# Performance work log

Measured on AMD Instinct MI355X. Metric: run time of the kernel, lower is better.

Reference implementation:

```python
import jax, jax.numpy as jnp
import numpy as np

B, T, D, H = 2, 2048, 1024, 16
DK = D // H


def setup_inputs() -> dict:
    key = jax.random.key(0)
    ks = jax.random.split(key, 12)
    q = jax.random.normal(ks[0], (B, T, D), jnp.float32)
    k = jax.random.normal(ks[1], (B, T, D), jnp.float32)
    v = jax.random.normal(ks[2], (B, T, D), jnp.float32)
    # padding mask [B,1,T]: 1 = valid, 0 = pad (nonzero per torch eq(0) semantics)
    lengths = jnp.array([T, (3 * T) // 4])
    mask = (jnp.arange(T)[None, None, :] < lengths[:, None, None]).astype(jnp.int32)
    s = 0.02
    Wq = jax.random.normal(ks[3], (D, D), jnp.float32) * s
    Wk = jax.random.normal(ks[4], (D, D), jnp.float32) * s
    Wv = jax.random.normal(ks[5], (D, D), jnp.float32) * s
    Wo = jax.random.normal(ks[6], (D, D), jnp.float32) * s
    bq = jnp.zeros((D,), jnp.float32)
    bk = jnp.zeros((D,), jnp.float32)
    bv = jnp.zeros((D,), jnp.float32)
    bo = jnp.zeros((D,), jnp.float32)
    return {"query": q, "key": k, "value": v, "mask": mask,
            "Wq": Wq, "bq": bq, "Wk": Wk, "bk": bk,
            "Wv": Wv, "bv": bv, "Wo": Wo, "bo": bo}


def reference(query, key, value, mask, Wq, bq, Wk, bk, Wv, bv, Wo, bo):
    # q,k,v projections -> [B, H, T, DK]
    def proj(x, W, b):
        return (x @ W.T + b).reshape(B, T, H, DK).transpose(0, 2, 1, 3)
    q = proj(query, Wq, bq)
    k = proj(key, Wk, bk)
    v = proj(value, Wv, bv)
    scores = jnp.einsum("bhqd,bhkd->bhqk", q, k) * (DK ** -0.5)  # [B,H,T,T]
    m = (mask == 0)[:, None, :, :]  # [B,1,1,T] broadcast over heads/queries
    scores = jnp.where(m, -jnp.inf, scores)
    attn = jax.nn.softmax(scores, axis=-1)
    attn = jnp.where(m, 0.0, attn)
    x = jnp.einsum("bhqk,bhkd->bhqd", attn, v)  # [B,H,T,DK]
    x = x.transpose(0, 2, 1, 3).reshape(B, T, D)
    return x @ Wo.T + bo
```

## Files before the change

### kernel.cpp

```cpp
#include <hip/hip_runtime.h>

typedef unsigned short u16;
typedef unsigned int u32;
typedef __bf16 bf16x8 __attribute__((ext_vector_type(8)));
typedef float floatx4 __attribute__((ext_vector_type(4)));

#define BB 2
#define TT 2048
#define DD 1024
#define HH 16
#define DKK 64
#define ACT (BB * TT * DD)
#define WTE (DD * DD)

__device__ inline u16 f2bf(float f) {
    union { float f; u32 u; } c; c.f = f;
    u32 r = (c.u + 0x7fffu + ((c.u >> 16) & 1u)) >> 16;
    return (u16)r;
}
__device__ inline u32 pack2bf(float a, float b) {
    return (u32)f2bf(a) | ((u32)f2bf(b) << 16);
}

typedef __attribute__((address_space(1))) const u32 gas_u32;
typedef __attribute__((address_space(3))) u32 las_u32;
__device__ __forceinline__ void gl2lds16(const u16* g, u16* l) {
    __builtin_amdgcn_global_load_lds((gas_u32*)g, (las_u32*)l, 16, 0, 0);
}

struct CvtArgs { const float* src[7]; u16* dst[7]; };
__global__ __launch_bounds__(256) void convert_bf16(CvtArgs a) {
    int bid = blockIdx.x, t, local;
    if (bid < 768) { t = bid >> 8; local = bid & 255; }
    else { int r = bid - 768; t = 3 + (r >> 6); local = r & 63; }
    const float* s = a.src[t];
    u16* d = a.dst[t];
    const int base = local * 16384;
    for (int i = 0; i < 8; i++) {
        const int idx = base + i * 2048 + threadIdx.x * 8;
        float4 x0 = *(const float4*)(s + idx);
        float4 x1 = *(const float4*)(s + idx + 4);
        uint4 p;
        p.x = pack2bf(x0.x, x0.y); p.y = pack2bf(x0.z, x0.w);
        p.z = pack2bf(x1.x, x1.y); p.w = pack2bf(x1.z, x1.w);
        *(uint4*)(d + idx) = p;
    }
}

__global__ __launch_bounds__(256) void qkv_gemm(
    const u16* __restrict__ Qc, const u16* __restrict__ Kc,
    const u16* __restrict__ Vc,
    const u16* __restrict__ Wqc, const u16* __restrict__ Wkc,
    const u16* __restrict__ Wvc,
    const float* __restrict__ bq, const float* __restrict__ bk,
    const float* __restrict__ bv,
    u16* __restrict__ ws)
{
    __shared__ __align__(16) u16 As[128 * 32];
    __shared__ __align__(16) u16 Bs[128 * 32];
    const int z = blockIdx.z;
    const u16* A = (z == 0) ? Qc : (z == 1) ? Kc : Vc;
    const u16* W = (z == 0) ? Wqc : (z == 1) ? Wkc : Wvc;
    const float* bias = (z == 0) ? bq : (z == 1) ? bk : bv;
    u16* out = ws + (size_t)z * (size_t)BB * HH * TT * DKK;

    const int tid  = threadIdx.x;
    const int wave = tid >> 6, lane = tid & 63;
    const int quad = lane >> 4, l16 = lane & 15;
    const int wm = wave & 1, wn = wave >> 1;
    const int m0 = blockIdx.y * 128, n0 = blockIdx.x * 128;
    const int K = DD;

    const int lrow = lane >> 2, lcol = (lane & 3) * 8;
    const u16* Ag0 = A + (size_t)(m0 + wave * 16 + lrow) * K + lcol;
    const u16* Ag1 = A + (size_t)(m0 + 64 + wave * 16 + lrow) * K + lcol;
    const u16* Wg0 = W + (size_t)(n0 + wave * 16 + lrow) * K + lcol;
    const u16* Wg1 = W + (size_t)(n0 + 64 + wave * 16 + lrow) * K + lcol;
    u16* AsD0 = &As[(wave * 16) * 32];
    u16* AsD1 = &As[(64 + wave * 16) * 32];
    u16* BsD0 = &Bs[(wave * 16) * 32];
    u16* BsD1 = &Bs[(64 + wave * 16) * 32];

    floatx4 acc[4][4];
    for (int i = 0; i < 4; i++)
        for (int j = 0; j < 4; j++)
            acc[i][j] = floatx4{0.f, 0.f, 0.f, 0.f};

    for (int k0 = 0; k0 < K; k0 += 32) {
        __syncthreads();
        gl2lds16(Ag0 + k0, AsD0);
        gl2lds16(Ag1 + k0, AsD1);
        gl2lds16(Wg0 + k0, BsD0);
        gl2lds16(Wg1 + k0, BsD1);
        __syncthreads();

        bf16x8 af[4], bfr[4];
        for (int mi = 0; mi < 4; mi++)
            af[mi] = *(const bf16x8*)&As[(wm * 64 + mi * 16 + l16) * 32 + quad * 8];
        for (int ni = 0; ni < 4; ni++)
            bfr[ni] = *(const bf16x8*)&Bs[(wn * 64 + ni * 16 + l16) * 32 + quad * 8];
        for (int mi = 0; mi < 4; mi++)
            for (int ni = 0; ni < 4; ni++)
                acc[mi][ni] = __builtin_amdgcn_mfma_f32_16x16x32_bf16(
                    af[mi], bfr[ni], acc[mi][ni], 0, 0, 0);
    }

    for (int ni = 0; ni < 4; ni++) {
        const int n = n0 + wn * 64 + ni * 16 + l16;
        const float bv2 = bias[n];
        for (int mi = 0; mi < 4; mi++) {
            for (int vv = 0; vv < 4; vv++) {
                const int m = m0 + wm * 64 + mi * 16 + quad * 4 + vv;
                const float val = acc[mi][ni][vv] + bv2;
                const int b = m >> 11, t = m & 2047, h = n >> 6, dk = n & 63;
                if (z == 2)
                    out[(((size_t)(b * HH + h)) * DKK + dk) * TT + t] = f2bf(val);
                else
                    out[(((size_t)(b * HH + h)) * TT + t) * DKK + dk] = f2bf(val);
            }
        }
    }
}

__global__ __launch_bounds__(256) void out_gemm(
    const u16* __restrict__ Av, const u16* __restrict__ Wv,
    const float* __restrict__ bias, float* __restrict__ outv)
{
    __shared__ __align__(16) u16 As[128 * 32];
    __shared__ __align__(16) u16 Bs[128 * 32];
    const int tid  = threadIdx.x;
    const int wave = tid >> 6, lane = tid & 63;
    const int quad = lane >> 4, l16 = lane & 15;
    const int wm = wave & 1, wn = wave >> 1;
    const int m0 = blockIdx.y * 128, n0 = blockIdx.x * 128;
    const int K = DD, N = DD;

    const int lrow = lane >> 2, lcol = (lane & 3) * 8;
    const u16* Ag0 = Av + (size_t)(m0 + wave * 16 + lrow) * K + lcol;
    const u16* Ag1 = Av + (size_t)(m0 + 64 + wave * 16 + lrow) * K + lcol;
    const u16* Wg0 = Wv + (size_t)(n0 + wave * 16 + lrow) * K + lcol;
    const u16* Wg1 = Wv + (size_t)(n0 + 64 + wave * 16 + lrow) * K + lcol;
    u16* AsD0 = &As[(wave * 16) * 32];
    u16* AsD1 = &As[(64 + wave * 16) * 32];
    u16* BsD0 = &Bs[(wave * 16) * 32];
    u16* BsD1 = &Bs[(64 + wave * 16) * 32];

    floatx4 acc[4][4];
    for (int i = 0; i < 4; i++)
        for (int j = 0; j < 4; j++)
            acc[i][j] = floatx4{0.f, 0.f, 0.f, 0.f};

    for (int k0 = 0; k0 < K; k0 += 32) {
        __syncthreads();
        gl2lds16(Ag0 + k0, AsD0);
        gl2lds16(Ag1 + k0, AsD1);
        gl2lds16(Wg0 + k0, BsD0);
        gl2lds16(Wg1 + k0, BsD1);
        __syncthreads();

        bf16x8 af[4], bfr[4];
        for (int mi = 0; mi < 4; mi++)
            af[mi] = *(const bf16x8*)&As[(wm * 64 + mi * 16 + l16) * 32 + quad * 8];
        for (int ni = 0; ni < 4; ni++)
            bfr[ni] = *(const bf16x8*)&Bs[(wn * 64 + ni * 16 + l16) * 32 + quad * 8];
        for (int mi = 0; mi < 4; mi++)
            for (int ni = 0; ni < 4; ni++)
                acc[mi][ni] = __builtin_amdgcn_mfma_f32_16x16x32_bf16(
                    af[mi], bfr[ni], acc[mi][ni], 0, 0, 0);
    }

    for (int ni = 0; ni < 4; ni++) {
        const int n = n0 + wn * 64 + ni * 16 + l16;
        const float bv2 = bias[n];
        for (int mi = 0; mi < 4; mi++)
            for (int vv = 0; vv < 4; vv++) {
                const int m = m0 + wm * 64 + mi * 16 + quad * 4 + vv;
                outv[(size_t)m * N + n] = acc[mi][ni][vv] + bv2;
            }
    }
}

__global__ __launch_bounds__(512) void attn_kernel(
    const u16* __restrict__ Qp, const u16* __restrict__ Kp,
    const u16* __restrict__ Vpt, const int* __restrict__ mask,
    u16* __restrict__ Xa)
{
    constexpr int LDK = 72, LDP = 72;
    __shared__ __align__(16) u16 Ks[64 * LDK];
    __shared__ __align__(16) u16 Vs[64 * LDK];
    __shared__ __align__(16) __bf16 Pl[8][16][LDP];
    const int tid  = threadIdx.x;
    const int wave = tid >> 6, lane = tid & 63;
    const int quad = lane >> 4, l16 = lane & 15;
    const int bid = blockIdx.x;
    const int qt = bid & 15, bh = bid >> 4;
    const int b = bh >> 4, h = bh & 15;
    const int qbase = qt * 128 + wave * 16;

    const u16* Qb = Qp + (size_t)bh * TT * DKK;
    const u16* Kb = Kp + (size_t)bh * TT * DKK;
    const u16* Vb = Vpt + (size_t)bh * DKK * TT;
    const int* mk = mask + b * TT;

    const int srow = tid >> 3, scol = (tid & 7) * 8;

    const bf16x8 qf0 = *(const bf16x8*)&Qb[(size_t)(qbase + l16) * DKK + quad * 8];
    const bf16x8 qf1 = *(const bf16x8*)&Qb[(size_t)(qbase + l16) * DKK + 32 + quad * 8];

    floatx4 o[4];
    float rsum[4];
    for (int i = 0; i < 4; i++) {
        o[i] = floatx4{0.f, 0.f, 0.f, 0.f};
        rsum[i] = 0.f;
    }

    uint4 kr = *(const uint4*)&Kb[(size_t)srow * DKK + scol];
    uint4 vr = *(const uint4*)&Vb[(size_t)srow * TT + scol];

    for (int ti = 0; ti < TT / 64; ti++) {
        const int k0 = ti * 64;
        __syncthreads();
        *(uint4*)&Ks[srow * LDK + scol] = kr;
        *(uint4*)&Vs[srow * LDK + scol] = vr;
        __syncthreads();
        if (ti + 1 < TT / 64) {
            kr = *(const uint4*)&Kb[(size_t)(k0 + 64 + srow) * DKK + scol];
            vr = *(const uint4*)&Vb[(size_t)srow * TT + k0 + 64 + scol];
        }

        const int mv0 = mk[k0 + l16];
        const int mv1 = mk[k0 + 16 + l16];
        const int mv2 = mk[k0 + 32 + l16];
        const int mv3 = mk[k0 + 48 + l16];
        if (!__any(mv0 | mv1 | mv2 | mv3)) continue;
        const float mf[4] = { mv0 ? 1.f : 0.f, mv1 ? 1.f : 0.f,
                              mv2 ? 1.f : 0.f, mv3 ? 1.f : 0.f };

        bf16x8 kf[4][2];
        for (int c = 0; c < 4; c++) {
            kf[c][0] = *(const bf16x8*)&Ks[(c * 16 + l16) * LDK + quad * 8];
            kf[c][1] = *(const bf16x8*)&Ks[(c * 16 + l16) * LDK + 32 + quad * 8];
        }

        floatx4 s[4];
        for (int c = 0; c < 4; c++) s[c] = floatx4{0.f, 0.f, 0.f, 0.f};
        for (int c = 0; c < 4; c++) {
            s[c] = __builtin_amdgcn_mfma_f32_16x16x32_bf16(qf0, kf[c][0], s[c], 0, 0, 0);
            s[c] = __builtin_amdgcn_mfma_f32_16x16x32_bf16(qf1, kf[c][1], s[c], 0, 0, 0);
        }

        for (int c = 0; c < 4; c++)
            for (int v = 0; v < 4; v++) {
                const float p = __expf(s[c][v] * 0.125f) * mf[c];
                rsum[v] += p;
                Pl[wave][quad * 4 + v][c * 16 + l16] = (__bf16)p;
            }

        __asm__ volatile("" ::: "memory");
        const bf16x8 pf0 = *(const bf16x8*)&Pl[wave][l16][quad * 8];
        const bf16x8 pf1 = *(const bf16x8*)&Pl[wave][l16][32 + quad * 8];
        __asm__ volatile("" ::: "memory");

        for (int nb = 0; nb < 4; nb++) {
            const bf16x8 vf0 = *(const bf16x8*)&Vs[(nb * 16 + l16) * LDK + quad * 8];
            const bf16x8 vf1 = *(const bf16x8*)&Vs[(nb * 16 + l16) * LDK + 32 + quad * 8];
            o[nb] = __builtin_amdgcn_mfma_f32_16x16x32_bf16(pf0, vf0, o[nb], 0, 0, 0);
            o[nb] = __builtin_amdgcn_mfma_f32_16x16x32_bf16(pf1, vf1, o[nb], 0, 0, 0);
        }
    }

    for (int off = 1; off < 16; off <<= 1)
        for (int v = 0; v < 4; v++)
            rsum[v] += __shfl_xor(rsum[v], off, 64);

    float inv[4];
    for (int v = 0; v < 4; v++) inv[v] = 1.0f / rsum[v];
    for (int nb = 0; nb < 4; nb++)
        for (int v = 0; v < 4; v++) {
            const int t = qbase + quad * 4 + v;
            Xa[((size_t)b * TT + t) * DD + h * DKK + nb * 16 + l16] =
                f2bf(o[nb][v] * inv[v]);
        }
}

extern "C" void kernel_launch(void* const* d_in, const int* in_sizes, int n_in,
                              void* d_out, int out_size, void* d_ws, size_t ws_size,
                              hipStream_t stream) {
    const float* q    = (const float*)d_in[0];
    const float* k    = (const float*)d_in[1];
    const float* v    = (const float*)d_in[2];
    const int*   mask = (const int*)d_in[3];
    const float* Wq   = (const float*)d_in[4];
    const float* bq   = (const float*)d_in[5];
    const float* Wk   = (const float*)d_in[6];
    const float* bk   = (const float*)d_in[7];
    const float* Wv   = (const float*)d_in[8];
    const float* bv   = (const float*)d_in[9];
    const float* Wo   = (const float*)d_in[10];
    const float* bo   = (const float*)d_in[11];

    u16* Qc  = (u16*)d_ws;
    u16* Kc  = Qc + (size_t)ACT;
    u16* Vc  = Kc + (size_t)ACT;
    u16* Wqc = Vc + (size_t)ACT;
    u16* Wkc = Wqc + (size_t)WTE;
    u16* Wvc = Wkc + (size_t)WTE;
    u16* Woc = Wvc + (size_t)WTE;
    u16* Qp  = Woc + (size_t)WTE;
    u16* Kp  = Qp + (size_t)ACT;
    u16* Vpt = Kp + (size_t)ACT;
    u16* Xa  = Vpt + (size_t)ACT;

    CvtArgs ca;
    ca.src[0] = q;  ca.dst[0] = Qc;
    ca.src[1] = k;  ca.dst[1] = Kc;
    ca.src[2] = v;  ca.dst[2] = Vc;
    ca.src[3] = Wq; ca.dst[3] = Wqc;
    ca.src[4] = Wk; ca.dst[4] = Wkc;
    ca.src[5] = Wv; ca.dst[5] = Wvc;
    ca.src[6] = Wo; ca.dst[6] = Woc;
    convert_bf16<<<1024, 256, 0, stream>>>(ca);

    qkv_gemm<<<dim3(DD / 128, (BB * TT) / 128, 3), 256, 0, stream>>>(
        Qc, Kc, Vc, Wqc, Wkc, Wvc, bq, bk, bv, Qp);

    attn_kernel<<<dim3(BB * HH * (TT / 128)), 512, 0, stream>>>(Qp, Kp, Vpt, mask, Xa);

    out_gemm<<<dim3(DD / 128, (BB * TT) / 128), 256, 0, stream>>>(Xa, Woc, bo, (float*)d_out);
}
```

Before: 247.0 us.

## Keep attention probabilities in registers via transposed QK^T and permlane swaps

Swaps the operands of the QK^T MFMA so each lane holds scores for one query across consecutive keys. The probabilities are then packed to bf16 with v_cvt_pk_bf16_f32 and redistributed with permlane32/permlane16 swaps into the A-operand layout for the PV MFMA. This removes the per-wave LDS staging buffer for P, its write/read round trip, and the per-row shuffle reductions. Fully valid tiles skip the per-element mask lookups, but the new row-sum bookkeeping and lane-swap correctness rest on subtle layout assumptions.

```diff
diff --git a/kernel.cpp b/kernel.cpp
--- a/kernel.cpp
+++ b/kernel.cpp
@@ -26,6 +26,20 @@
 typedef __attribute__((address_space(3))) u32 las_u32;
 __device__ __forceinline__ void gl2lds16(const u16* g, u16* l) {
     __builtin_amdgcn_global_load_lds((gas_u32*)g, (las_u32*)l, 16, 0, 0);
+}
+
+__device__ __forceinline__ u32 cvtpk_bf16(float lo, float hi) {
+    u32 r;
+    asm("v_cvt_pk_bf16_f32 %0, %1, %2" : "=v"(r) : "v"(lo), "v"(hi));
+    return r;
+}
+
+__device__ __forceinline__ void quad_gather(u32 &a, u32 &b) {
+    asm volatile("s_nop 1\n\t"
+                 "v_permlane32_swap_b32 %0, %1\n\t"
+                 "s_nop 1\n\t"
+                 "v_permlane16_swap_b32 %0, %1"
+                 : "+v"(a), "+v"(b));
 }
 
 struct CvtArgs { const float* src[7]; u16* dst[7]; };
@@ -185,10 +199,9 @@
     const u16* __restrict__ Vpt, const int* __restrict__ mask,
     u16* __restrict__ Xa)
 {
-    constexpr int LDK = 72, LDP = 72;
+    constexpr int LDK = 72;
     __shared__ __align__(16) u16 Ks[64 * LDK];
     __shared__ __align__(16) u16 Vs[64 * LDK];
-    __shared__ __align__(16) __bf16 Pl[8][16][LDP];
     const int tid  = threadIdx.x;
     const int wave = tid >> 6, lane = tid & 63;
     const int quad = lane >> 4, l16 = lane & 15;
@@ -208,11 +221,8 @@
     const bf16x8 qf1 = *(const bf16x8*)&Qb[(size_t)(qbase + l16) * DKK + 32 + quad * 8];
 
     floatx4 o[4];
-    float rsum[4];
-    for (int i = 0; i < 4; i++) {
-        o[i] = floatx4{0.f, 0.f, 0.f, 0.f};
-        rsum[i] = 0.f;
-    }
+    for (int i = 0; i < 4; i++) o[i] = floatx4{0.f, 0.f, 0.f, 0.f};
+    float rs = 0.f;
 
     uint4 kr = *(const uint4*)&Kb[(size_t)srow * DKK + scol];
     uint4 vr = *(const uint4*)&Vb[(size_t)srow * TT + scol];
@@ -233,49 +243,76 @@
         const int mv2 = mk[k0 + 32 + l16];
         const int mv3 = mk[k0 + 48 + l16];
         if (!__any(mv0 | mv1 | mv2 | mv3)) continue;
-        const float mf[4] = { mv0 ? 1.f : 0.f, mv1 ? 1.f : 0.f,
-                              mv2 ? 1.f : 0.f, mv3 ? 1.f : 0.f };
+        const bool allv = __all(mv0 && mv1 && mv2 && mv3);
 
         bf16x8 kf[4][2];
+        #pragma unroll
         for (int c = 0; c < 4; c++) {
             kf[c][0] = *(const bf16x8*)&Ks[(c * 16 + l16) * LDK + quad * 8];
             kf[c][1] = *(const bf16x8*)&Ks[(c * 16 + l16) * LDK + 32 + quad * 8];
         }
 
         floatx4 s[4];
+        #pragma unroll
         for (int c = 0; c < 4; c++) s[c] = floatx4{0.f, 0.f, 0.f, 0.f};
+        #pragma unroll
         for (int c = 0; c < 4; c++) {
-            s[c] = __builtin_amdgcn_mfma_f32_16x16x32_bf16(qf0, kf[c][0], s[c], 0, 0, 0);
-            s[c] = __builtin_amdgcn_mfma_f32_16x16x32_bf16(qf1, kf[c][1], s[c], 0, 0, 0);
-        }
-
+            s[c] = __builtin_amdgcn_mfma_f32_16x16x32_bf16(kf[c][0], qf0, s[c], 0, 0, 0);
+            s[c] = __builtin_amdgcn_mfma_f32_16x16x32_bf16(kf[c][1], qf1, s[c], 0, 0, 0);
+        }
+
+        float p[4][4];
+        if (allv) {
+            #pragma unroll
+            for (int c = 0; c < 4; c++)
+                #pragma unroll
+                for (int v = 0; v < 4; v++)
+                    p[c][v] = __expf(s[c][v] * 0.125f);
+        } else {
+            #pragma unroll
+            for (int c = 0; c < 4; c++)
+                #pragma unroll
+                for (int v = 0; v < 4; v++)
+                    p[c][v] = mk[k0 + c * 16 + quad * 4 + v]
+                                  ? __expf(s[c][v] * 0.125f) : 0.f;
+        }
+        #pragma unroll
         for (int c = 0; c < 4; c++)
-            for (int v = 0; v < 4; v++) {
-                const float p = __expf(s[c][v] * 0.125f) * mf[c];
-                rsum[v] += p;
-                Pl[wave][quad * 4 + v][c * 16 + l16] = (__bf16)p;
-            }
-
-        __asm__ volatile("" ::: "memory");
-        const bf16x8 pf0 = *(const bf16x8*)&Pl[wave][l16][quad * 8];
-        const bf16x8 pf1 = *(const bf16x8*)&Pl[wave][l16][32 + quad * 8];
-        __asm__ volatile("" ::: "memory");
-
+            #pragma unroll
+            for (int v = 0; v < 4; v++)
+                rs += p[c][v];
+
+        u32 A0 = cvtpk_bf16(p[0][0], p[0][1]), B0 = cvtpk_bf16(p[1][0], p[1][1]);
+        u32 A1 = cvtpk_bf16(p[0][2], p[0][3]), B1 = cvtpk_bf16(p[1][2], p[1][3]);
+        u32 A2 = cvtpk_bf16(p[2][0], p[2][1]), B2 = cvtpk_bf16(p[3][0], p[3][1]);
+        u32 A3 = cvtpk_bf16(p[2][2], p[2][3]), B3 = cvtpk_bf16(p[3][2], p[3][3]);
+        quad_gather(A0, B0);
+        quad_gather(A1, B1);
+        quad_gather(A2, B2);
+        quad_gather(A3, B3);
+        union { u32 w[4]; bf16x8 v; } pa0, pa1;
+        pa0.w[0] = A0; pa0.w[1] = A1; pa0.w[2] = B0; pa0.w[3] = B1;
+        pa1.w[0] = A2; pa1.w[1] = A3; pa1.w[2] = B2; pa1.w[3] = B3;
+
+        #pragma unroll
         for (int nb = 0; nb < 4; nb++) {
             const bf16x8 vf0 = *(const bf16x8*)&Vs[(nb * 16 + l16) * LDK + quad * 8];
             const bf16x8 vf1 = *(const bf16x8*)&Vs[(nb * 16 + l16) * LDK + 32 + quad * 8];
-            o[nb] = __builtin_amdgcn_mfma_f32_16x16x32_bf16(pf0, vf0, o[nb], 0, 0, 0);
-            o[nb] = __builtin_amdgcn_mfma_f32_16x16x32_bf16(pf1, vf1, o[nb], 0, 0, 0);
-        }
-    }
-
-    for (int off = 1; off < 16; off <<= 1)
-        for (int v = 0; v < 4; v++)
-            rsum[v] += __shfl_xor(rsum[v], off, 64);
-
+            o[nb] = __builtin_amdgcn_mfma_f32_16x16x32_bf16(pa0.v, vf0, o[nb], 0, 0, 0);
+            o[nb] = __builtin_amdgcn_mfma_f32_16x16x32_bf16(pa1.v, vf1, o[nb], 0, 0, 0);
+        }
+    }
+
+    rs += __shfl_xor(rs, 16, 64);
+    rs += __shfl_xor(rs, 32, 64);
     float inv[4];
-    for (int v = 0; v < 4; v++) inv[v] = 1.0f / rsum[v];
+    #pragma unroll
+    for (int v = 0; v < 4; v++)
+        inv[v] = 1.0f / __shfl(rs, quad * 4 + v, 64);
+
+    #pragma unroll
     for (int nb = 0; nb < 4; nb++)
+        #pragma unroll
         for (int v = 0; v < 4; v++) {
             const int t = qbase + quad * 4 + v;
             Xa[((size_t)b * TT + t) * DD + h * DKK + nb * 16 + l16] =
```

After: 236.6 us. 1.04x faster.
